# Kernel tuning notes

Measured on AMD Instinct MI355X. Metric: run time of the kernel, lower is better.

## Reference

```python
import jax, jax.numpy as jnp
import numpy as np

HEADS = 16
D_MODEL = 1024
D_FF = 4096
D_K = D_MODEL // HEADS
EPS = 1e-5


def layer_norm(x, g, b):
    mu = jnp.mean(x, axis=-1, keepdims=True)
    var = jnp.mean(jnp.square(x - mu), axis=-1, keepdims=True)
    return (x - mu) * jax.lax.rsqrt(var + EPS) * g + b


def setup_inputs() -> dict:
    key = jax.random.key(0)
    ks = jax.random.split(key, 12)
    B, S = 2, 2048
    s = 0.02
    return {
        "x": jax.random.normal(ks[0], (B, S, D_MODEL), jnp.float32),
        "mask": jnp.zeros((B, 1, 1, S), jnp.bool_),
        "W_Q": jax.random.normal(ks[1], (D_MODEL, D_MODEL), jnp.float32) * s,
        "W_K": jax.random.normal(ks[2], (D_MODEL, D_MODEL), jnp.float32) * s,
        "W_V": jax.random.normal(ks[3], (D_MODEL, D_MODEL), jnp.float32) * s,
        "W_O": jax.random.normal(ks[4], (D_MODEL, D_MODEL), jnp.float32) * s,
        "W1": jax.random.normal(ks[5], (D_FF, D_MODEL), jnp.float32) * s,
        "b1": jnp.zeros((D_FF,), jnp.float32),
        "W2": jax.random.normal(ks[6], (D_MODEL, D_FF), jnp.float32) * s,
        "b2": jnp.zeros((D_MODEL,), jnp.float32),
        "g1": jnp.ones((D_MODEL,), jnp.float32),
        "beta1": jnp.zeros((D_MODEL,), jnp.float32),
        "g2": jnp.ones((D_MODEL,), jnp.float32),
        "beta2": jnp.zeros((D_MODEL,), jnp.float32),
    }


def reference(x, mask, W_Q, W_K, W_V, W_O, W1, b1, W2, b2, g1, beta1, g2, beta2):
    B, S, _ = x.shape
    # pre-LN block (pre_ln=True)
    res = x
    h = layer_norm(x, g1, beta1)
    # torch Linear: y = h @ W.T
    q = (h @ W_Q.T).reshape(B, S, HEADS, D_K).transpose(0, 2, 1, 3)  # [B,H,S,dk]
    k = (h @ W_K.T).reshape(B, S, HEADS, D_K).transpose(0, 2, 1, 3)
    v = (h @ W_V.T).reshape(B, S, HEADS, D_K).transpose(0, 2, 1, 3)
    e = jnp.einsum("bhqd,bhkd->bhqk", q, k) / jnp.sqrt(jnp.float32(D_K))
    e = jnp.where(mask, -jnp.inf, e)
    w = jax.nn.softmax(e, axis=-1)
    a = jnp.einsum("bhqk,bhkd->bhqd", w, v)
    a = a.transpose(0, 2, 1, 3).reshape(B, S, D_MODEL)
    o = a @ W_O.T
    x = o + res  # dropout identity in eval
    # FFN sub-block
    res = x
    h = layer_norm(x, g2, beta2)
    # faithful to source: Linear -> Linear -> ReLU (ReLU at the end)
    f = jax.nn.relu((h @ W1.T + b1) @ W2.T + b2)
    return f + res
```

## Files before the change

kernel.cpp:

```cpp
#include <hip/hip_runtime.h>

typedef __attribute__((ext_vector_type(8))) short short8;
typedef __attribute__((ext_vector_type(4))) float f32x4;

typedef const void __attribute__((address_space(1)))* gas_ptr;
typedef void __attribute__((address_space(3)))* las_ptr;

__device__ __forceinline__ void gl16(const void* g, void* l) {
    __builtin_amdgcn_global_load_lds((gas_ptr)g, (las_ptr)l, 16, 0, 0);
}

__device__ __forceinline__ unsigned short f2bf(float f) {
    union { float f; unsigned u; } v; v.f = f;
    unsigned r = v.u + 0x7FFFu + ((v.u >> 16) & 1u);
    return (unsigned short)(r >> 16);
}
__device__ __forceinline__ float exp2_fast(float x) {
    float r; asm("v_exp_f32 %0, %1" : "=v"(r) : "v"(x)); return r;
}
__device__ __forceinline__ unsigned cvtpk(float lo, float hi) {
    unsigned r; asm("v_cvt_pk_bf16_f32 %0, %1, %2" : "=v"(r) : "v"(lo), "v"(hi)); return r;
}

#define QSCALE 0.18033688011112042f

__global__ __launch_bounds__(256) void cvt_kernel(const float* __restrict__ in,
                                                  unsigned short* __restrict__ out,
                                                  int n4) {
    int i = blockIdx.x * blockDim.x + threadIdx.x;
    int stride = gridDim.x * blockDim.x;
    for (; i < n4; i += stride) {
        float4 v = ((const float4*)in)[i];
        ushort4 o;
        o.x = f2bf(v.x); o.y = f2bf(v.y); o.z = f2bf(v.z); o.w = f2bf(v.w);
        ((ushort4*)out)[i] = o;
    }
}

__global__ __launch_bounds__(256) void ln_kernel(const float* __restrict__ x,
                                                 const float* __restrict__ g,
                                                 const float* __restrict__ bta,
                                                 unsigned short* __restrict__ out) {
    const int row = blockIdx.x, t = threadIdx.x;
    const float4 v = ((const float4*)(x + (size_t)row * 1024))[t];
    float s  = v.x + v.y + v.z + v.w;
    float s2 = v.x * v.x + v.y * v.y + v.z * v.z + v.w * v.w;
    for (int m = 1; m <= 32; m <<= 1) {
        s  += __shfl_xor(s, m);
        s2 += __shfl_xor(s2, m);
    }
    __shared__ float red[8];
    const int wid = t >> 6, lane = t & 63;
    if (lane == 0) { red[wid] = s; red[4 + wid] = s2; }
    __syncthreads();
    s  = red[0] + red[1] + red[2] + red[3];
    s2 = red[4] + red[5] + red[6] + red[7];
    const float mu  = s * (1.0f / 1024.0f);
    const float var = s2 * (1.0f / 1024.0f) - mu * mu;
    const float r   = rsqrtf(var + 1e-5f);
    const float4 gv = ((const float4*)g)[t];
    const float4 bv = ((const float4*)bta)[t];
    ushort4 o;
    o.x = f2bf((v.x - mu) * r * gv.x + bv.x);
    o.y = f2bf((v.y - mu) * r * gv.y + bv.y);
    o.z = f2bf((v.z - mu) * r * gv.z + bv.z);
    o.w = f2bf((v.w - mu) * r * gv.w + bv.w);
    ((ushort4*)(out + (size_t)row * 1024))[t] = o;
}

template <int EPI, int BN>
__global__ __launch_bounds__(256) void gemm_bt(const unsigned short* __restrict__ A,
                                               const unsigned short* __restrict__ B,
                                               const float* __restrict__ bias,
                                               const float* __restrict__ res,
                                               void* __restrict__ out,
                                               int M, int N, int K) {
    __shared__ unsigned short As[128 * 64];
    __shared__ unsigned short Bs[BN * 64];
    const int t = threadIdx.x;
    const int m0 = blockIdx.x * 128, n0 = blockIdx.y * BN;
    const int lane = t & 63, wid = t >> 6;
    const int wr = wid >> 1, wc = wid & 1;
    const int fr = lane & 15, fq = lane >> 4;
    const int NJ = BN / 32;
    const int NBJ = BN / 32;

    f32x4 acc[4][NJ] = {};

    const int srow = t >> 3;
    const int lelem = ((t & 7) ^ (srow & 7)) << 3;
    size_t aoff[4], boff[NBJ];
#pragma unroll
    for (int j = 0; j < 4; ++j)
        aoff[j] = (size_t)(m0 + srow + j * 32) * K + lelem;
#pragma unroll
    for (int j = 0; j < NBJ; ++j)
        boff[j] = (size_t)(n0 + srow + j * 32) * K + lelem;

    const int swz = (fr & 7) << 4;
    const char* abase = (const char*)As + (wr * 64 + fr) * 128;
    const char* bbase = (const char*)Bs + (wc * (BN / 2) + fr) * 128;

    for (int k0 = 0; k0 < K; k0 += 64) {
#pragma unroll
        for (int j = 0; j < 4; ++j)
            gl16(&A[aoff[j] + k0], &As[(t + j * 256) * 8]);
#pragma unroll
        for (int j = 0; j < NBJ; ++j)
            gl16(&B[boff[j] + k0], &Bs[(t + j * 256) * 8]);
        __syncthreads();
#pragma unroll
        for (int kk = 0; kk < 2; ++kk) {
            const int ib = ((kk << 6) | (fq << 4)) ^ swz;
            short8 af[4], bf[NJ];
#pragma unroll
            for (int i = 0; i < 4; ++i)
                af[i] = *(const short8*)(abase + i * 16 * 128 + ib);
#pragma unroll
            for (int j = 0; j < NJ; ++j)
                bf[j] = *(const short8*)(bbase + j * 16 * 128 + ib);
#pragma unroll
            for (int i = 0; i < 4; ++i)
#pragma unroll
                for (int j = 0; j < NJ; ++j)
                    acc[i][j] = __builtin_amdgcn_mfma_f32_16x16x32_bf16(af[i], bf[j], acc[i][j], 0, 0, 0);
        }
        __syncthreads();
    }

#pragma unroll
    for (int i = 0; i < 4; ++i)
#pragma unroll
        for (int j = 0; j < NJ; ++j)
#pragma unroll
            for (int q = 0; q < 4; ++q) {
                const int row = m0 + wr * 64 + i * 16 + fq * 4 + q;
                const int col = n0 + wc * (BN / 2) + j * 16 + fr;
                const size_t idx = (size_t)row * N + col;
                float v = acc[i][j][q];
                if (EPI == 0) {
                    ((unsigned short*)out)[idx] = f2bf(v);
                } else if (EPI == 1) {
                    ((unsigned short*)out)[idx] = f2bf(v + bias[col]);
                } else if (EPI == 2) {
                    ((float*)out)[idx] = v + res[idx];
                } else if (EPI == 3) {
                    float u = v + bias[col];
                    u = u > 0.0f ? u : 0.0f;
                    ((float*)out)[idx] = u + res[idx];
                } else {
                    ((unsigned short*)out)[idx] = f2bf(col < 1024 ? v * QSCALE : v);
                }
            }
}

__global__ __launch_bounds__(256, 2) void attn_kernel(const unsigned short* __restrict__ qk,
                                                      const unsigned short* __restrict__ vt,
                                                      unsigned short* __restrict__ out) {
    __shared__ unsigned short Kls[2][2048];
    __shared__ unsigned short Vls[2][2048];

    const int t = threadIdx.x, lane = t & 63, w = t >> 6;
    const int fr = lane & 15, fq = lane >> 4;
    const int flat = blockIdx.x;
    const int xcd = flat & 7, slot = flat >> 3;
    const int bh = xcd * 4 + (slot >> 4);
    const int qx = slot & 15;
    const int b = bh >> 4, h = bh & 15;
    const size_t tokbase = (size_t)b * 2048;
    const int q0 = qx * 128 + w * 32;

    short8 qf[2][2];
#pragma unroll
    for (int qt = 0; qt < 2; ++qt)
#pragma unroll
        for (int c = 0; c < 2; ++c)
            qf[qt][c] = *(const short8*)&qk[(tokbase + q0 + qt * 16 + fr) * 2048 + h * 64 + c * 32 + fq * 8];

    const int krow = t >> 3;
    const int kcolb = ((t & 7) << 4) ^ ((krow & 7) << 4);
    const unsigned short* ksrc = qk + (tokbase + krow) * 2048 + 1024 + h * 64 + (kcolb >> 1);
    const unsigned short* vsrc = vt + (size_t)(h * 64 + (t >> 2)) * 4096 + tokbase + (t & 3) * 8;

    const int sw = (fr & 7) << 4;
    const int kb0 = fr * 128 + ((fq * 16) ^ sw);
    const int vb0 = fr * 64 + fq * 16;

    f32x4 acc[2][4] = {};
    float lrun[2] = {0.0f, 0.0f};

    auto stage = [&](int kv, int buf) {
        gl16(ksrc + (size_t)kv * 2048, &Kls[buf][t * 8]);
        gl16(vsrc + kv, &Vls[buf][t * 8]);
    };

    stage(0, 0);
    __syncthreads();

    int cur = 0;
    for (int kv0 = 0; kv0 < 2048; kv0 += 32) {
        if (kv0 + 32 < 2048) stage(kv0 + 32, cur ^ 1);

        const char* kbase = (const char*)&Kls[cur][0];
        const char* vbase = (const char*)&Vls[cur][0];
        short8 ka[2][2], vf[4];
#pragma unroll
        for (int kh = 0; kh < 2; ++kh)
#pragma unroll
            for (int c = 0; c < 2; ++c)
                ka[kh][c] = *(const short8*)(kbase + kh * 2048 + (kb0 ^ (c * 64)));
#pragma unroll
        for (int dt = 0; dt < 4; ++dt)
            vf[dt] = *(const short8*)(vbase + dt * 1024 + vb0);

#pragma unroll
        for (int qt = 0; qt < 2; ++qt) {
            f32x4 e0 = {}, e1 = {};
            e0 = __builtin_amdgcn_mfma_f32_16x16x32_bf16(ka[0][0], qf[qt][0], e0, 0, 0, 0);
            e0 = __builtin_amdgcn_mfma_f32_16x16x32_bf16(ka[0][1], qf[qt][1], e0, 0, 0, 0);
            e1 = __builtin_amdgcn_mfma_f32_16x16x32_bf16(ka[1][0], qf[qt][0], e1, 0, 0, 0);
            e1 = __builtin_amdgcn_mfma_f32_16x16x32_bf16(ka[1][1], qf[qt][1], e1, 0, 0, 0);

            float p[8];
#pragma unroll
            for (int i = 0; i < 4; ++i) {
                p[i]     = exp2_fast(e0[i]);
                p[4 + i] = exp2_fast(e1[i]);
            }
            lrun[qt] += ((p[0] + p[1]) + (p[2] + p[3])) + ((p[4] + p[5]) + (p[6] + p[7]));

            const unsigned w0 = cvtpk(p[0], p[1]);
            const unsigned w1 = cvtpk(p[2], p[3]);
            const unsigned w2 = cvtpk(p[4], p[5]);
            const unsigned w3 = cvtpk(p[6], p[7]);
            const int s0 = ((fq & 1) << 5) + fr;
            const int s1 = s0 + 16;
            const unsigned a0 = __shfl(w0, s0), a1 = __shfl(w1, s0);
            const unsigned a2 = __shfl(w0, s1), a3 = __shfl(w1, s1);
            const unsigned b0 = __shfl(w2, s0), b1 = __shfl(w3, s0);
            const unsigned b2 = __shfl(w2, s1), b3 = __shfl(w3, s1);
            union { unsigned u[4]; short8 s; } pu;
            const bool lohalf = (fq < 2);
            pu.u[0] = lohalf ? a0 : b0;
            pu.u[1] = lohalf ? a1 : b1;
            pu.u[2] = lohalf ? a2 : b2;
            pu.u[3] = lohalf ? a3 : b3;
            const short8 pf = pu.s;
#pragma unroll
            for (int dt = 0; dt < 4; ++dt)
                acc[qt][dt] = __builtin_amdgcn_mfma_f32_16x16x32_bf16(pf, vf[dt], acc[qt][dt], 0, 0, 0);
        }

        asm volatile("s_waitcnt vmcnt(0)");
        __syncthreads();
        cur ^= 1;
    }

#pragma unroll
    for (int qt = 0; qt < 2; ++qt) {
        float lr = lrun[qt];
        lr += __shfl_xor(lr, 16);
        lr += __shfl_xor(lr, 32);
        const float linv = 1.0f / lr;
        float li[4];
#pragma unroll
        for (int i = 0; i < 4; ++i) li[i] = __shfl(linv, fq * 4 + i);
#pragma unroll
        for (int dt = 0; dt < 4; ++dt)
#pragma unroll
            for (int i = 0; i < 4; ++i)
                out[(tokbase + q0 + qt * 16 + fq * 4 + i) * 1024 + h * 64 + dt * 16 + fr] =
                    f2bf(acc[qt][dt][i] * li[i]);
    }
}

extern "C" void kernel_launch(void* const* d_in, const int* in_sizes, int n_in,
                              void* d_out, int out_size, void* d_ws, size_t ws_size,
                              hipStream_t stream) {
    const float* x     = (const float*)d_in[0];
    const float* W_Q   = (const float*)d_in[2];
    const float* W_K   = (const float*)d_in[3];
    const float* W_V   = (const float*)d_in[4];
    const float* W_O   = (const float*)d_in[5];
    const float* W1    = (const float*)d_in[6];
    const float* b1    = (const float*)d_in[7];
    const float* W2    = (const float*)d_in[8];
    const float* b2    = (const float*)d_in[9];
    const float* g1    = (const float*)d_in[10];
    const float* beta1 = (const float*)d_in[11];
    const float* g2    = (const float*)d_in[12];
    const float* beta2 = (const float*)d_in[13];

    const int TOK = 4096, DM = 1024, DFF = 4096;

    unsigned short* wsu = (unsigned short*)d_ws;
    unsigned short* wq  = wsu;
    unsigned short* wk  = wq + 1048576;
    unsigned short* wv  = wk + 1048576;
    unsigned short* wo  = wv + 1048576;
    unsigned short* w1  = wo + 1048576;
    unsigned short* w2  = w1 + 4194304;
    unsigned short* hln = w2 + 4194304;
    unsigned short* qkb = hln + 4194304;
    unsigned short* vt  = qkb + 8388608;
    unsigned short* ab  = vt + 4194304;
    float* x1           = (float*)(ab + 4194304);
    unsigned short* t1  = (unsigned short*)(x1 + 4194304);

    cvt_kernel<<<1024, 256, 0, stream>>>(W_Q, wq, 1048576 / 4);
    cvt_kernel<<<1024, 256, 0, stream>>>(W_K, wk, 1048576 / 4);
    cvt_kernel<<<1024, 256, 0, stream>>>(W_V, wv, 1048576 / 4);
    cvt_kernel<<<1024, 256, 0, stream>>>(W_O, wo, 1048576 / 4);
    cvt_kernel<<<2048, 256, 0, stream>>>(W1, w1, 4194304 / 4);
    cvt_kernel<<<2048, 256, 0, stream>>>(W2, w2, 4194304 / 4);

    ln_kernel<<<TOK, 256, 0, stream>>>(x, g1, beta1, hln);

    gemm_bt<4, 128><<<dim3(TOK / 128, 2048 / 128), 256, 0, stream>>>(hln, wq, nullptr, nullptr, qkb, TOK, 2048, DM);
    gemm_bt<0, 64><<<dim3(DM / 128, TOK / 64), 256, 0, stream>>>(wv, hln, nullptr, nullptr, vt, DM, TOK, DM);

    attn_kernel<<<512, 256, 0, stream>>>(qkb, vt, ab);

    gemm_bt<2, 64><<<dim3(TOK / 128, DM / 64), 256, 0, stream>>>(ab, wo, nullptr, x, x1, TOK, DM, DM);

    ln_kernel<<<TOK, 256, 0, stream>>>(x1, g2, beta2, hln);

    gemm_bt<1, 128><<<dim3(TOK / 128, DFF / 128), 256, 0, stream>>>(hln, w1, b1, nullptr, t1, TOK, DFF, DM);
    gemm_bt<3, 64><<<dim3(TOK / 128, DM / 64), 256, 0, stream>>>(t1, w2, b2, x1, d_out, TOK, DM, DFF);
}
```

Baseline: 260.8 us.

## Double-buffer GEMM LDS tiles and use one barrier per iteration

The GEMM kernel gets two LDS buffers for its A and B tiles. The next K tile is issued with global_load_lds while MFMAs run on the current tile, replacing the load-sync-compute-sync pattern. Both the GEMM and attention loops now use a single combined waitcnt+barrier at the top of each iteration instead of two syncs. This doubles LDS use per GEMM block, which can lower occupancy, and relies on a single barrier being enough to prevent overwriting a buffer that is still being read.

```diff
diff --git a/kernel.cpp b/kernel.cpp
--- a/kernel.cpp
+++ b/kernel.cpp
@@ -8,6 +8,13 @@
 
 __device__ __forceinline__ void gl16(const void* g, void* l) {
     __builtin_amdgcn_global_load_lds((gas_ptr)g, (las_ptr)l, 16, 0, 0);
+}
+
+__device__ __forceinline__ void tile_barrier() {
+    __builtin_amdgcn_sched_barrier(0);
+    asm volatile("s_waitcnt vmcnt(0)" ::: "memory");
+    __builtin_amdgcn_s_barrier();
+    __builtin_amdgcn_sched_barrier(0);
 }
 
 __device__ __forceinline__ unsigned short f2bf(float f) {
@@ -75,8 +82,8 @@
                                                const float* __restrict__ res,
                                                void* __restrict__ out,
                                                int M, int N, int K) {
-    __shared__ unsigned short As[128 * 64];
-    __shared__ unsigned short Bs[BN * 64];
+    __shared__ unsigned short As[2][128 * 64];
+    __shared__ unsigned short Bs[2][BN * 64];
     const int t = threadIdx.x;
     const int m0 = blockIdx.x * 128, n0 = blockIdx.y * BN;
     const int lane = t & 63, wid = t >> 6;
@@ -97,18 +104,26 @@
     for (int j = 0; j < NBJ; ++j)
         boff[j] = (size_t)(n0 + srow + j * 32) * K + lelem;
 
+    auto stage = [&](int k0, int buf) {
+#pragma unroll
+        for (int j = 0; j < 4; ++j)
+            gl16(&A[aoff[j] + k0], &As[buf][(t + j * 256) * 8]);
+#pragma unroll
+        for (int j = 0; j < NBJ; ++j)
+            gl16(&B[boff[j] + k0], &Bs[buf][(t + j * 256) * 8]);
+    };
+
     const int swz = (fr & 7) << 4;
-    const char* abase = (const char*)As + (wr * 64 + fr) * 128;
-    const char* bbase = (const char*)Bs + (wc * (BN / 2) + fr) * 128;
-
+    const int arow = (wr * 64 + fr) * 128;
+    const int brow = (wc * (BN / 2) + fr) * 128;
+
+    stage(0, 0);
+    int buf = 0;
     for (int k0 = 0; k0 < K; k0 += 64) {
-#pragma unroll
-        for (int j = 0; j < 4; ++j)
-            gl16(&A[aoff[j] + k0], &As[(t + j * 256) * 8]);
-#pragma unroll
-        for (int j = 0; j < NBJ; ++j)
-            gl16(&B[boff[j] + k0], &Bs[(t + j * 256) * 8]);
-        __syncthreads();
+        tile_barrier();
+        if (k0 + 64 < K) stage(k0 + 64, buf ^ 1);
+        const char* abase = (const char*)&As[buf][0] + arow;
+        const char* bbase = (const char*)&Bs[buf][0] + brow;
 #pragma unroll
         for (int kk = 0; kk < 2; ++kk) {
             const int ib = ((kk << 6) | (fq << 4)) ^ swz;
@@ -125,7 +140,7 @@
                 for (int j = 0; j < NJ; ++j)
                     acc[i][j] = __builtin_amdgcn_mfma_f32_16x16x32_bf16(af[i], bf[j], acc[i][j], 0, 0, 0);
         }
-        __syncthreads();
+        buf ^= 1;
     }
 
 #pragma unroll
@@ -195,10 +210,9 @@
     };
 
     stage(0, 0);
-    __syncthreads();
-
     int cur = 0;
     for (int kv0 = 0; kv0 < 2048; kv0 += 32) {
+        tile_barrier();
         if (kv0 + 32 < 2048) stage(kv0 + 32, cur ^ 1);
 
         const char* kbase = (const char*)&Kls[cur][0];
@@ -250,9 +264,6 @@
             for (int dt = 0; dt < 4; ++dt)
                 acc[qt][dt] = __builtin_amdgcn_mfma_f32_16x16x32_bf16(pf, vf[dt], acc[qt][dt], 0, 0, 0);
         }
-
-        asm volatile("s_waitcnt vmcnt(0)");
-        __syncthreads();
         cur ^= 1;
     }
 
```

Result: faster. 251.8 us (-3.5%).
